# Performance work log

Measured on AMD Instinct MI355X. Metric: run time of the kernel, lower is better.

## Reference

```python
import jax, jax.numpy as jnp
import numpy as np

NEG = -1000000000.0


def setup_inputs() -> dict:
    key = jax.random.key(0)
    k1, k2, k3, k4, k5 = jax.random.split(key, 5)
    B, T, D, Q = 8, 2048, 1024, 128
    x = jax.random.normal(k1, (B, T, D), dtype=jnp.float32)
    attn_mask = jax.random.randint(k2, (B, T), 0, 2).astype(jnp.bool_)
    s = 1.0 / np.sqrt(D)
    Wq = jax.random.normal(k3, (Q, D), dtype=jnp.float32) * s
    Wk = jax.random.normal(k4, (Q, D), dtype=jnp.float32) * s
    Wv = jax.random.normal(k5, (Q, D), dtype=jnp.float32) * s
    return {"x": x, "attn_mask": attn_mask, "Wq": Wq, "Wk": Wk, "Wv": Wv}


def reference(x, attn_mask, Wq, Wk, Wv):
    # x: (B,T,D); W*: (Q,D) torch Linear weights (y = x @ W.T)
    q = jnp.einsum('btd,qd->btq', x, Wq)
    k = jnp.einsum('btd,qd->btq', x, Wk)
    v = jnp.einsum('btd,qd->btq', x, Wv)
    logits = jnp.einsum('btq,bsq->bts', q, k)  # (B,T,T), no 1/sqrt(d) scaling (matches source)
    m = attn_mask[:, None, :]  # (B,1,T) broadcasts over query dim, == repeat(1,T,1)
    logits = jnp.where(m, logits, NEG)
    A = jax.nn.softmax(logits, axis=-1)
    A = jnp.where(m, A, 0.0)
    return jnp.einsum('bts,bsq->btq', A, v)
```

## Files before the change

### kernel.cpp

```cpp
#include <hip/hip_runtime.h>
#include <hip/hip_bf16.h>
#include <hip/hip_fp16.h>

typedef _Float16 half8 __attribute__((ext_vector_type(8)));
typedef _Float16 half4v __attribute__((ext_vector_type(4)));
typedef float float4v __attribute__((ext_vector_type(4)));

#define MFMA_F16(a, b, c) __builtin_amdgcn_mfma_f32_16x16x32_f16((a), (b), (c), 0, 0, 0)

#define GLDS16(gp, lp) \
    __builtin_amdgcn_global_load_lds((const __attribute__((address_space(1))) unsigned int*)(gp), \
                                     (__attribute__((address_space(3))) unsigned int*)(lp), 16, 0, 0)

#define BATCH 8
#define SEQ   2048
#define DIM   1024
#define QD    128
#define BT    (BATCH * SEQ)
#define NSPLIT 4
#define KSPAN (SEQ / NSPLIT)

__device__ __forceinline__ float dpp_max16(float x) {
    int v;
    v = __builtin_amdgcn_update_dpp(0, __float_as_int(x), 0xB1, 0xF, 0xF, false);
    x = fmaxf(x, __int_as_float(v));
    v = __builtin_amdgcn_update_dpp(0, __float_as_int(x), 0x4E, 0xF, 0xF, false);
    x = fmaxf(x, __int_as_float(v));
    v = __builtin_amdgcn_update_dpp(0, __float_as_int(x), 0x141, 0xF, 0xF, false);
    x = fmaxf(x, __int_as_float(v));
    v = __builtin_amdgcn_update_dpp(0, __float_as_int(x), 0x140, 0xF, 0xF, false);
    x = fmaxf(x, __int_as_float(v));
    return x;
}

__global__ __launch_bounds__(256) void cvt_w_kernel(const float* __restrict__ Wq,
                                                    const float* __restrict__ Wk,
                                                    const float* __restrict__ Wv,
                                                    _Float16* __restrict__ Wh) {
    const float* src = (blockIdx.y == 0) ? Wq : ((blockIdx.y == 1) ? Wk : Wv);
    int i = blockIdx.x * 256 + threadIdx.x;
    float4 f = ((const float4*)src)[i];
    half4v h = {(_Float16)f.x, (_Float16)f.y, (_Float16)f.z, (_Float16)f.w};
    ((half4v*)(Wh + (size_t)blockIdx.y * QD * DIM))[i] = h;
}

__global__ __launch_bounds__(512, 4) void proj_kernel(
    const float* __restrict__ x,
    const _Float16* __restrict__ Wh,
    _Float16* __restrict__ q_out,
    _Float16* __restrict__ k_out,
    _Float16* __restrict__ vt_out)
{
    __shared__ _Float16 As[2][64 * 64];
    __shared__ _Float16 Bs[2][192 * 64];

    const int tid  = threadIdx.x;
    const int lane = tid & 63;
    const int wave = tid >> 6;
    const int quad = lane >> 4;
    const int l15  = lane & 15;
    const int wr   = wave >> 2;
    const int wcg  = wave & 3;

    const int row0 = blockIdx.x * 64;
    const int ch   = blockIdx.y;

    const int ar  = tid >> 3;
    const int ac8 = tid & 7;
    const float* xp = x + (size_t)(row0 + ar) * DIM + ac8 * 8;
    const int aslot = ar * 64 + ((ac8 ^ (ar & 7)) * 8);

    float4v acc[2][3];
#pragma unroll
    for (int rf = 0; rf < 2; rf++)
#pragma unroll
        for (int nf = 0; nf < 3; nf++)
            acc[rf][nf] = (float4v){0.f, 0.f, 0.f, 0.f};

    {
        float4 a0 = *(const float4*)(xp + 0);
        float4 a1 = *(const float4*)(xp + 4);
#pragma unroll
        for (int c = 0; c < 3; c++) {
            int ci = c * 512 + tid;
            int ri = ci >> 3;
            int m  = ri >> 6;
            int wrow = ch * 64 + (ri & 63);
            int g  = (ci & 7) ^ (ri & 7);
            GLDS16(Wh + (size_t)m * QD * DIM + (size_t)wrow * DIM + g * 8, &Bs[0][ci * 8]);
        }
        half8 h;
        h[0] = (_Float16)a0.x; h[1] = (_Float16)a0.y; h[2] = (_Float16)a0.z; h[3] = (_Float16)a0.w;
        h[4] = (_Float16)a1.x; h[5] = (_Float16)a1.y; h[6] = (_Float16)a1.z; h[7] = (_Float16)a1.w;
        *(half8*)&As[0][aslot] = h;
    }
    __syncthreads();

    for (int t = 0; t < 16; t++) {
        const int cur = t & 1;
        const int nxt = cur ^ 1;

        float4 b0, b1;
        if (t < 15) {
            const float* xq = xp + (t + 1) * 64;
            b0 = *(const float4*)(xq + 0);
            b1 = *(const float4*)(xq + 4);
            const int kkn = (t + 1) * 64;
#pragma unroll
            for (int c = 0; c < 3; c++) {
                int ci = c * 512 + tid;
                int ri = ci >> 3;
                int m  = ri >> 6;
                int wrow = ch * 64 + (ri & 63);
                int g  = (ci & 7) ^ (ri & 7);
                GLDS16(Wh + (size_t)m * QD * DIM + (size_t)wrow * DIM + kkn + g * 8,
                       &Bs[nxt][ci * 8]);
            }
        }

        half8 af[2][2];
#pragma unroll
        for (int rf = 0; rf < 2; rf++)
#pragma unroll
            for (int kc = 0; kc < 2; kc++) {
                int r = wr * 32 + rf * 16 + l15;
                int g = (kc * 4 + quad) ^ (r & 7);
                af[rf][kc] = *(const half8*)&As[cur][r * 64 + g * 8];
            }
        half8 bf[3][2];
#pragma unroll
        for (int nf = 0; nf < 3; nf++)
#pragma unroll
            for (int kc = 0; kc < 2; kc++) {
                int r = wcg * 48 + nf * 16 + l15;
                int g = (kc * 4 + quad) ^ (r & 7);
                bf[nf][kc] = *(const half8*)&Bs[cur][r * 64 + g * 8];
            }
#pragma unroll
        for (int kc = 0; kc < 2; kc++)
#pragma unroll
            for (int rf = 0; rf < 2; rf++)
#pragma unroll
                for (int nf = 0; nf < 3; nf++)
                    acc[rf][nf] = MFMA_F16(af[rf][kc], bf[nf][kc], acc[rf][nf]);

        if (t < 15) {
            half8 h;
            h[0] = (_Float16)b0.x; h[1] = (_Float16)b0.y; h[2] = (_Float16)b0.z; h[3] = (_Float16)b0.w;
            h[4] = (_Float16)b1.x; h[5] = (_Float16)b1.y; h[6] = (_Float16)b1.z; h[7] = (_Float16)b1.w;
            *(half8*)&As[nxt][aslot] = h;
            __syncthreads();
        }
    }

#pragma unroll
    for (int rf = 0; rf < 2; rf++) {
        int grow0 = row0 + wr * 32 + rf * 16 + quad * 4;
        int b  = grow0 >> 11;
        int t0 = grow0 & 2047;
#pragma unroll
        for (int nf = 0; nf < 3; nf++) {
            int col192 = wcg * 48 + nf * 16 + l15;
            int m   = col192 >> 6;
            int col = ch * 64 + (col192 & 63);
            if (m == 2) {
                half4v h;
#pragma unroll
                for (int r = 0; r < 4; r++) h[r] = (_Float16)acc[rf][nf][r];
                *(half4v*)&vt_out[((size_t)(b * QD + col)) * SEQ + t0] = h;
            } else {
                _Float16* out = (m == 0) ? q_out : k_out;
#pragma unroll
                for (int r = 0; r < 4; r++)
                    out[(size_t)(grow0 + r) * QD + col] = (_Float16)acc[rf][nf][r];
            }
        }
    }
}

__global__ __launch_bounds__(256, 2) void attn_kernel(
    const _Float16* __restrict__ q,
    const _Float16* __restrict__ k,
    const _Float16* __restrict__ vt,
    const int* __restrict__ mask,
    _Float16* __restrict__ Op,
    float2* __restrict__ ml)
{
    __shared__ _Float16 Ks[64 * 128];
    __shared__ _Float16 Vs[128 * 64];
    __shared__ _Float16 Ps[4 * 32 * 64];
    __shared__ float Msf[64];

    const int tid  = threadIdx.x;
    const int lane = tid & 63;
    const int wave = tid >> 6;
    const int quad = lane >> 4;
    const int l15  = lane & 15;

    const int b  = blockIdx.y;
    const int z  = blockIdx.z;
    const int rowbase = blockIdx.x * 128 + wave * 32;

    half8 qf[2][4];
#pragma unroll
    for (int rf = 0; rf < 2; rf++) {
        const _Float16* qrow = q + ((size_t)(b * SEQ + rowbase + rf * 16 + l15)) * QD + quad * 8;
#pragma unroll
        for (int kc = 0; kc < 4; kc++)
            qf[rf][kc] = *(const half8*)(qrow + kc * 32);
    }

    const half8 onesv = {(_Float16)1, (_Float16)1, (_Float16)1, (_Float16)1,
                         (_Float16)1, (_Float16)1, (_Float16)1, (_Float16)1};

    float4v oacc[2][8];
#pragma unroll
    for (int rf = 0; rf < 2; rf++)
#pragma unroll
        for (int n = 0; n < 8; n++)
            oacc[rf][n] = (float4v){0.f, 0.f, 0.f, 0.f};
    float4v lacc[2] = {(float4v){0.f, 0.f, 0.f, 0.f}, (float4v){0.f, 0.f, 0.f, 0.f}};
    float mrow[2][4];
#pragma unroll
    for (int rf = 0; rf < 2; rf++)
#pragma unroll
        for (int r = 0; r < 4; r++) mrow[rf][r] = -1e30f;

    _Float16* Pw = &Ps[wave * 32 * 64];

    for (int sb = z * KSPAN; sb < z * KSPAN + KSPAN; sb += 64) {
        __syncthreads();
#pragma unroll
        for (int c = 0; c < 4; c++) {
            int ci = wave * 256 + c * 64 + lane;
            int r  = ci >> 4;
            int gs = ci & 15;
            int g  = (gs & 8) | ((gs ^ r) & 7);
            GLDS16(k + ((size_t)(b * SEQ + sb + r)) * QD + g * 8, &Ks[(wave * 256 + c * 64) * 8]);
        }
#pragma unroll
        for (int c = 0; c < 4; c++) {
            int ci = wave * 256 + c * 64 + lane;
            int r  = ci >> 3;
            int g  = ((ci & 7) ^ r) & 7;
            GLDS16(vt + ((size_t)(b * QD + r)) * SEQ + sb + g * 8, &Vs[(wave * 256 + c * 64) * 8]);
        }
        if (tid < 64) Msf[tid] = mask[b * SEQ + sb + tid] ? 0.f : -1e30f;
        __syncthreads();

        float4v sacc[2][4];
#pragma unroll
        for (int rf = 0; rf < 2; rf++)
#pragma unroll
            for (int j = 0; j < 4; j++)
                sacc[rf][j] = (float4v){0.f, 0.f, 0.f, 0.f};
#pragma unroll
        for (int kc = 0; kc < 4; kc++) {
            half8 kf[4];
#pragma unroll
            for (int j = 0; j < 4; j++) {
                int r  = j * 16 + l15;
                int g  = kc * 4 + quad;
                int gs = (g & 8) | ((g ^ r) & 7);
                kf[j] = *(const half8*)&Ks[r * 128 + gs * 8];
            }
#pragma unroll
            for (int rf = 0; rf < 2; rf++)
#pragma unroll
                for (int j = 0; j < 4; j++)
                    sacc[rf][j] = MFMA_F16(qf[rf][kc], kf[j], sacc[rf][j]);
        }

        float alpha[2][4];
#pragma unroll
        for (int rf = 0; rf < 2; rf++) {
            float rmax[4] = {-1e30f, -1e30f, -1e30f, -1e30f};
#pragma unroll
            for (int j = 0; j < 4; j++) {
                float bias = Msf[j * 16 + l15];
#pragma unroll
                for (int r = 0; r < 4; r++) {
                    float s = sacc[rf][j][r] + bias;
                    sacc[rf][j][r] = s;
                    rmax[r] = fmaxf(rmax[r], s);
                }
            }
#pragma unroll
            for (int r = 0; r < 4; r++) {
                float rm = dpp_max16(rmax[r]);
                float mnew = fmaxf(mrow[rf][r], rm);
                alpha[rf][r] = __expf(mrow[rf][r] - mnew);
                mrow[rf][r] = mnew;
            }
        }

#pragma unroll
        for (int rf = 0; rf < 2; rf++)
#pragma unroll
            for (int j = 0; j < 4; j++) {
                int col = j * 16 + l15;
                int gc  = col >> 3;
#pragma unroll
                for (int r = 0; r < 4; r++) {
                    int m  = rf * 16 + quad * 4 + r;
                    int gs = (gc ^ m) & 7;
                    float p = __expf(sacc[rf][j][r] - mrow[rf][r]);
                    Pw[m * 64 + gs * 8 + (col & 7)] = (_Float16)p;
                }
            }

#pragma unroll
        for (int rf = 0; rf < 2; rf++) {
#pragma unroll
            for (int n = 0; n < 8; n++)
#pragma unroll
                for (int r = 0; r < 4; r++)
                    oacc[rf][n][r] *= alpha[rf][r];
#pragma unroll
            for (int r = 0; r < 4; r++) lacc[rf][r] *= alpha[rf][r];
        }

#pragma unroll
        for (int kc = 0; kc < 2; kc++) {
            half8 pf[2];
#pragma unroll
            for (int rf = 0; rf < 2; rf++) {
                int m  = rf * 16 + l15;
                int gs = ((kc * 4 + quad) ^ m) & 7;
                pf[rf] = *(const half8*)&Pw[m * 64 + gs * 8];
            }
#pragma unroll
            for (int n = 0; n < 8; n++) {
                int r  = n * 16 + l15;
                int gs = ((kc * 4 + quad) ^ r) & 7;
                half8 vf = *(const half8*)&Vs[r * 64 + gs * 8];
#pragma unroll
                for (int rf = 0; rf < 2; rf++)
                    oacc[rf][n] = MFMA_F16(pf[rf], vf, oacc[rf][n]);
            }
#pragma unroll
            for (int rf = 0; rf < 2; rf++)
                lacc[rf] = MFMA_F16(pf[rf], onesv, lacc[rf]);
        }
    }

    _Float16* Oz = Op + (size_t)z * BT * QD;
#pragma unroll
    for (int rf = 0; rf < 2; rf++) {
#pragma unroll
        for (int n = 0; n < 8; n++) {
            int col = n * 16 + l15;
#pragma unroll
            for (int r = 0; r < 4; r++) {
                int row = rowbase + rf * 16 + quad * 4 + r;
                Oz[((size_t)(b * SEQ + row)) * QD + col] = (_Float16)oacc[rf][n][r];
            }
        }
        if (l15 == 0) {
#pragma unroll
            for (int r = 0; r < 4; r++) {
                int row = rowbase + rf * 16 + quad * 4 + r;
                ml[(size_t)z * BT + b * SEQ + row] = make_float2(mrow[rf][r], lacc[rf][r]);
            }
        }
    }
}

__global__ __launch_bounds__(256) void merge_kernel(
    const _Float16* __restrict__ Op,
    const float2* __restrict__ ml,
    float* __restrict__ out)
{
    int gid = blockIdx.x * 256 + threadIdx.x;
    int row = gid >> 4;
    int c8  = (gid & 15) * 8;

    float2 a[NSPLIT];
    float m = -3.0e38f;
#pragma unroll
    for (int s = 0; s < NSPLIT; s++) { a[s] = ml[(size_t)s * BT + row]; m = fmaxf(m, a[s].x); }
    float sc[NSPLIT];
    float denom = 0.f;
#pragma unroll
    for (int s = 0; s < NSPLIT; s++) { sc[s] = __expf(a[s].x - m); denom += sc[s] * a[s].y; }
    float inv = (denom > 0.f) ? (1.0f / denom) : 0.f;

    float acc[8] = {0, 0, 0, 0, 0, 0, 0, 0};
#pragma unroll
    for (int s = 0; s < NSPLIT; s++) {
        half8 o = *(const half8*)&Op[(size_t)s * BT * QD + (size_t)row * QD + c8];
#pragma unroll
        for (int e = 0; e < 8; e++) acc[e] += (float)o[e] * sc[s];
    }
    float4 lo = make_float4(acc[0] * inv, acc[1] * inv, acc[2] * inv, acc[3] * inv);
    float4 hi = make_float4(acc[4] * inv, acc[5] * inv, acc[6] * inv, acc[7] * inv);
    *(float4*)&out[(size_t)row * QD + c8] = lo;
    *(float4*)&out[(size_t)row * QD + c8 + 4] = hi;
}

extern "C" void kernel_launch(void* const* d_in, const int* in_sizes, int n_in,
                              void* d_out, int out_size, void* d_ws, size_t ws_size,
                              hipStream_t stream) {
    const float* x    = (const float*)d_in[0];
    const int*   mask = (const int*)d_in[1];
    const float* Wq   = (const float*)d_in[2];
    const float* Wk   = (const float*)d_in[3];
    const float* Wv   = (const float*)d_in[4];
    float* out = (float*)d_out;

    char* p = (char*)d_ws;
    _Float16* Wh  = (_Float16*)p; p += (size_t)3 * QD * DIM * 2;
    _Float16* qb  = (_Float16*)p; p += (size_t)BT * QD * 2;
    _Float16* kb  = (_Float16*)p; p += (size_t)BT * QD * 2;
    _Float16* vtb = (_Float16*)p; p += (size_t)BT * QD * 2;
    _Float16* Op  = (_Float16*)p; p += (size_t)NSPLIT * BT * QD * 2;
    float2*   ml  = (float2*)p;

    cvt_w_kernel<<<dim3(QD * DIM / 4 / 256, 3), 256, 0, stream>>>(Wq, Wk, Wv, Wh);
    proj_kernel<<<dim3(BT / 64, 2), 512, 0, stream>>>(x, Wh, qb, kb, vtb);
    attn_kernel<<<dim3(SEQ / 128, BATCH, NSPLIT), 256, 0, stream>>>(qb, kb, vtb, mask, Op, ml);
    merge_kernel<<<dim3(BT * 16 / 256), 256, 0, stream>>>(Op, ml, out);
}
```

Measured before the change: 155.2 us.

## Add lazy softmax rescaling, MFMA priority hints, and XCD-aware block remapping

The attention kernel now rescales the output accumulators only when some row's block maximum exceeds the running maximum by more than a threshold of 3. Otherwise it keeps a stale maximum and fixes it up once at the end using the true maximum it tracks alongside. MFMA sections in both the projection and attention kernels are wrapped in s_setprio raises. Attention blocks are remapped so that blocks sharing the same batch and split land on the same XCD, for better L2 reuse of K/V. The risk is fp16 overflow of P when the stale maximum lags, since exp can reach e^3, plus extra index arithmetic.

```diff
diff --git a/kernel.cpp b/kernel.cpp
--- a/kernel.cpp
+++ b/kernel.cpp
@@ -136,6 +136,7 @@
                 int g = (kc * 4 + quad) ^ (r & 7);
                 bf[nf][kc] = *(const half8*)&Bs[cur][r * 64 + g * 8];
             }
+        __builtin_amdgcn_s_setprio(1);
 #pragma unroll
         for (int kc = 0; kc < 2; kc++)
 #pragma unroll
@@ -143,6 +144,7 @@
 #pragma unroll
                 for (int nf = 0; nf < 3; nf++)
                     acc[rf][nf] = MFMA_F16(af[rf][kc], bf[nf][kc], acc[rf][nf]);
+        __builtin_amdgcn_s_setprio(0);
 
         if (t < 15) {
             half8 h;
@@ -197,9 +199,14 @@
     const int quad = lane >> 4;
     const int l15  = lane & 15;
 
-    const int b  = blockIdx.y;
-    const int z  = blockIdx.z;
-    const int rowbase = blockIdx.x * 128 + wave * 32;
+    const int lin = blockIdx.x + 16 * (blockIdx.y + 8 * blockIdx.z);
+    const int xcd = lin & 7;
+    const int idx = lin >> 3;
+    const int yz  = xcd * 4 + (idx >> 4);
+    const int wx  = idx & 15;
+    const int b   = yz & 7;
+    const int z   = yz >> 3;
+    const int rowbase = wx * 128 + wave * 32;
 
     half8 qf[2][4];
 #pragma unroll
@@ -221,10 +228,11 @@
             oacc[rf][n] = (float4v){0.f, 0.f, 0.f, 0.f};
     float4v lacc[2] = {(float4v){0.f, 0.f, 0.f, 0.f}, (float4v){0.f, 0.f, 0.f, 0.f}};
     float mrow[2][4];
+    float mtrue[2][4];
 #pragma unroll
     for (int rf = 0; rf < 2; rf++)
 #pragma unroll
-        for (int r = 0; r < 4; r++) mrow[rf][r] = -1e30f;
+        for (int r = 0; r < 4; r++) { mrow[rf][r] = -1e30f; mtrue[rf][r] = -1e30f; }
 
     _Float16* Pw = &Ps[wave * 32 * 64];
 
@@ -254,6 +262,7 @@
 #pragma unroll
             for (int j = 0; j < 4; j++)
                 sacc[rf][j] = (float4v){0.f, 0.f, 0.f, 0.f};
+        __builtin_amdgcn_s_setprio(1);
 #pragma unroll
         for (int kc = 0; kc < 4; kc++) {
             half8 kf[4];
@@ -270,8 +279,10 @@
                 for (int j = 0; j < 4; j++)
                     sacc[rf][j] = MFMA_F16(qf[rf][kc], kf[j], sacc[rf][j]);
         }
-
-        float alpha[2][4];
+        __builtin_amdgcn_s_setprio(0);
+
+        float rmv[2][4];
+        bool ok = true;
 #pragma unroll
         for (int rf = 0; rf < 2; rf++) {
             float rmax[4] = {-1e30f, -1e30f, -1e30f, -1e30f};
@@ -288,10 +299,24 @@
 #pragma unroll
             for (int r = 0; r < 4; r++) {
                 float rm = dpp_max16(rmax[r]);
-                float mnew = fmaxf(mrow[rf][r], rm);
-                alpha[rf][r] = __expf(mrow[rf][r] - mnew);
-                mrow[rf][r] = mnew;
-            }
+                rmv[rf][r] = rm;
+                mtrue[rf][r] = fmaxf(mtrue[rf][r], rm);
+                ok = ok && (rm <= mrow[rf][r] + 3.0f);
+            }
+        }
+        if (!__all(ok)) {
+#pragma unroll
+            for (int rf = 0; rf < 2; rf++)
+#pragma unroll
+                for (int r = 0; r < 4; r++) {
+                    float mnew = fmaxf(mrow[rf][r], rmv[rf][r]);
+                    float a = __expf(mrow[rf][r] - mnew);
+                    mrow[rf][r] = mnew;
+#pragma unroll
+                    for (int n = 0; n < 8; n++)
+                        oacc[rf][n][r] *= a;
+                    lacc[rf][r] *= a;
+                }
         }
 
 #pragma unroll
@@ -309,17 +334,7 @@
                 }
             }
 
-#pragma unroll
-        for (int rf = 0; rf < 2; rf++) {
-#pragma unroll
-            for (int n = 0; n < 8; n++)
-#pragma unroll
-                for (int r = 0; r < 4; r++)
-                    oacc[rf][n][r] *= alpha[rf][r];
-#pragma unroll
-            for (int r = 0; r < 4; r++) lacc[rf][r] *= alpha[rf][r];
-        }
-
+        __builtin_amdgcn_s_setprio(1);
 #pragma unroll
         for (int kc = 0; kc < 2; kc++) {
             half8 pf[2];
@@ -342,7 +357,17 @@
             for (int rf = 0; rf < 2; rf++)
                 lacc[rf] = MFMA_F16(pf[rf], onesv, lacc[rf]);
         }
-    }
+        __builtin_amdgcn_s_setprio(0);
+    }
+
+    float fin[2][4];
+#pragma unroll
+    for (int rf = 0; rf < 2; rf++)
+#pragma unroll
+        for (int r = 0; r < 4; r++) {
+            fin[rf][r] = __expf(mrow[rf][r] - mtrue[rf][r]);
+            lacc[rf][r] *= fin[rf][r];
+        }
 
     _Float16* Oz = Op + (size_t)z * BT * QD;
 #pragma unroll
@@ -353,14 +378,14 @@
 #pragma unroll
             for (int r = 0; r < 4; r++) {
                 int row = rowbase + rf * 16 + quad * 4 + r;
-                Oz[((size_t)(b * SEQ + row)) * QD + col] = (_Float16)oacc[rf][n][r];
+                Oz[((size_t)(b * SEQ + row)) * QD + col] = (_Float16)(oacc[rf][n][r] * fin[rf][r]);
             }
         }
         if (l15 == 0) {
 #pragma unroll
             for (int r = 0; r < 4; r++) {
                 int row = rowbase + rf * 16 + quad * 4 + r;
-                ml[(size_t)z * BT + b * SEQ + row] = make_float2(mrow[rf][r], lacc[rf][r]);
+                ml[(size_t)z * BT + b * SEQ + row] = make_float2(mtrue[rf][r], lacc[rf][r]);
             }
         }
     }
```

Result: no change. 156.7 us (+1.0%).
